# Optimization experiments

Hardware: AMD Instinct MI355X
Metric: run time of the kernel (lower is better)

Reference implementation:

```python
import jax, jax.numpy as jnp
import numpy as np

NUM_ITERS = 3


def squash(s):
    # s: [..., V]
    sq = (s ** 2).sum(-1, keepdims=True)
    return sq * s / ((1.0 + sq) * jnp.sqrt(sq))


def setup_inputs() -> dict:
    key = jax.random.key(0)
    kx, kw = jax.random.split(key)
    B, O, I, V, D = 32, 1, 4096, 512, 8
    x = jax.random.normal(kx, (B, I, D), dtype=jnp.float32)
    W = 0.01 * jax.random.normal(kw, (O, I, V, D), dtype=jnp.float32)
    return {"x": x, "W": W}


def reference(x, W):
    B = x.shape[0]
    O, I, V, _ = W.shape
    # x_hat[b,o,i,v] = sum_d W[o,i,v,d] * x[b,i,d]
    x_hat = jnp.einsum('oivd,bid->boiv', W, x)  # [B,O,I,V]
    x_hat_d = jax.lax.stop_gradient(x_hat)

    b = jnp.zeros((B, O, I), dtype=x.dtype)
    for it in range(NUM_ITERS):
        c = jax.nn.softmax(b, axis=1)  # over out caps
        if it == NUM_ITERS - 1:
            outputs = squash((c[:, :, :, None] * x_hat).sum(-2, keepdims=True))
        else:
            outputs = squash((c[:, :, :, None] * x_hat_d).sum(-2, keepdims=True))
            b = b + (outputs * x_hat_d).sum(-1)

    outputs = outputs.squeeze(-2)  # [B,O,V]
    # decode_idx == -1 branch
    classes = jax.nn.softmax(jnp.sqrt((outputs ** 2).sum(2)), axis=1)  # [B,O]
    max_idx = jnp.argmax(classes, axis=1)  # [B]
    masked = jax.nn.one_hot(max_idx, O, dtype=outputs.dtype)  # [B,O]
    t = (outputs * masked[:, :, None]).sum(axis=1)[:, None, :]  # [B,1,V]
    return (t, outputs)
```

## Files before the change

kernel.cpp:

```cpp
#include <hip/hip_runtime.h>
#include <stdint.h>


#define NB 32
#define NI 4096
#define NV 512
#define ND 8
#define NK 32768
#define KB 128
#define KSB (NK / KB)
#define KSW 16
#define NG (KB / 8)

typedef __fp16 f16x8 __attribute__((ext_vector_type(8)));
typedef __fp16 f16x2 __attribute__((ext_vector_type(2)));
typedef float  f32x16 __attribute__((ext_vector_type(16)));

__global__ __launch_bounds__(256) void x_prep(
    const float* __restrict__ x, __fp16* __restrict__ xh,
    __fp16* __restrict__ xl)
{
    const int tid = blockIdx.x * 256 + threadIdx.x;
    const int b = tid & 31;
    const int g = tid >> 5;

    const float4* xp = (const float4*)(x + (size_t)b * NK + (size_t)g * 8);
    const float4 f0 = xp[0];
    const float4 f1 = xp[1];

    const f16x2 h0 = __builtin_amdgcn_cvt_pkrtz(f0.x, f0.y);
    const f16x2 h1 = __builtin_amdgcn_cvt_pkrtz(f0.z, f0.w);
    const f16x2 h2 = __builtin_amdgcn_cvt_pkrtz(f1.x, f1.y);
    const f16x2 h3 = __builtin_amdgcn_cvt_pkrtz(f1.z, f1.w);
    const f16x2 l0 = __builtin_amdgcn_cvt_pkrtz(f0.x - (float)h0.x, f0.y - (float)h0.y);
    const f16x2 l1 = __builtin_amdgcn_cvt_pkrtz(f0.z - (float)h1.x, f0.w - (float)h1.y);
    const f16x2 l2 = __builtin_amdgcn_cvt_pkrtz(f1.x - (float)h2.x, f1.y - (float)h2.y);
    const f16x2 l3 = __builtin_amdgcn_cvt_pkrtz(f1.z - (float)h3.x, f1.w - (float)h3.y);

    const f16x8 h = {h0.x, h0.y, h1.x, h1.y, h2.x, h2.y, h3.x, h3.y};
    const f16x8 l = {l0.x, l0.y, l1.x, l1.y, l2.x, l2.y, l3.x, l3.y};
    ((f16x8*)xh)[tid] = h;
    ((f16x8*)xl)[tid] = l;
}

__global__ __launch_bounds__(1024) void caps_mfma(
    const float* __restrict__ W, const __fp16* __restrict__ xh,
    const __fp16* __restrict__ xl, __fp16* __restrict__ partial_h)
{
    const int t    = threadIdx.x;
    const int lane = t & 63;
    const int wave = t >> 6;
    const int half = lane >> 5;
    const int ln32 = lane & 31;

    const int kb = blockIdx.x & (KB - 1);
    const int vg = blockIdx.x >> 7;
    const int v0 = vg * 32;
    const int k0 = kb * KSB + wave * KSW;
    const int g0 = (k0 >> 3) + half;

    const __fp16* ah = xh + ((size_t)g0 * 32 + ln32) * 8;
    const __fp16* al = xl + ((size_t)g0 * 32 + ln32) * 8;
    const float4* wp = (const float4*)(W + ((size_t)g0 * NV + v0 + ln32) * ND);

    const float4 w0 = wp[0];
    const float4 w1 = wp[1];
    const f16x8 a_hi = *(const f16x8*)ah;
    const f16x8 a_lo = *(const f16x8*)al;

    const f16x2 h01 = __builtin_amdgcn_cvt_pkrtz(w0.x, w0.y);
    const f16x2 h23 = __builtin_amdgcn_cvt_pkrtz(w0.z, w0.w);
    const f16x2 h45 = __builtin_amdgcn_cvt_pkrtz(w1.x, w1.y);
    const f16x2 h67 = __builtin_amdgcn_cvt_pkrtz(w1.z, w1.w);
    const f16x8 b = {h01.x, h01.y, h23.x, h23.y, h45.x, h45.y, h67.x, h67.y};

    f32x16 acc;
#pragma unroll
    for (int r = 0; r < 16; ++r) acc[r] = 0.0f;
    acc = __builtin_amdgcn_mfma_f32_32x32x16_f16(a_hi, b, acc, 0, 0, 0);
    acc = __builtin_amdgcn_mfma_f32_32x32x16_f16(a_lo, b, acc, 0, 0, 0);

    __shared__ float red[16 * 1024];
#pragma unroll
    for (int r = 0; r < 16; ++r)
        red[wave * 1024 + r * 64 + lane] = acc[r];
    __syncthreads();

    float val = 0.0f;
#pragma unroll
    for (int w = 0; w < 16; ++w)
        val += red[w * 1024 + t];

    const int r  = t >> 6;
    const int ln = t & 63;
    const int row = (r & 3) + 8 * (r >> 2) + 4 * (ln >> 5);
    const int col = ln & 31;
    partial_h[((size_t)kb * NB + row) * NV + v0 + col] = (__fp16)val;
}

__global__ __launch_bounds__(256) void caps_reduce8(
    const __fp16* __restrict__ partial_h, float* __restrict__ partial2)
{
    const int t = threadIdx.x;
    const int b = blockIdx.x & 31;
    const int g = blockIdx.x >> 5;

    const __fp16* p = partial_h + ((size_t)(g * 8) * NB + b) * NV + 2 * t;
    float s0 = 0.0f, s1 = 0.0f;
#pragma unroll
    for (int j = 0; j < 8; ++j) {
        const f16x2 h = *(const f16x2*)(p + (size_t)j * NB * NV);
        s0 += (float)h.x;
        s1 += (float)h.y;
    }

    float2 o = {s0, s1};
    ((float2*)(partial2 + ((size_t)g * NB + b) * NV))[t] = o;
}

__global__ __launch_bounds__(512) void caps_finish(
    const float* __restrict__ partial2, float* __restrict__ out)
{
    const int v = threadIdx.x;
    const int b = blockIdx.x;

    float s = 0.0f;
#pragma unroll
    for (int g = 0; g < NG; ++g)
        s += partial2[((size_t)g * NB + b) * NV + v];

    float sq = s * s;
#pragma unroll
    for (int off = 32; off > 0; off >>= 1)
        sq += __shfl_xor(sq, off, 64);

    __shared__ float red[8];
    if ((v & 63) == 0) red[v >> 6] = sq;
    __syncthreads();
    float tot = 0.0f;
#pragma unroll
    for (int wv = 0; wv < 8; ++wv) tot += red[wv];

    const float factor = sqrtf(tot) / (1.0f + tot);
    const float r = s * factor;

    out[(size_t)b * NV + v]           = r;
    out[NB * NV + (size_t)b * NV + v] = r;
}

extern "C" void kernel_launch(void* const* d_in, const int* in_sizes, int n_in,
                              void* d_out, int out_size, void* d_ws, size_t ws_size,
                              hipStream_t stream) {
    const float* x = (const float*)d_in[0];
    const float* W = (const float*)d_in[1];
    float* out     = (float*)d_out;

    __fp16* xh       = (__fp16*)d_ws;
    __fp16* xl       = xh + (size_t)NB * NK;
    __fp16* partialh = xl + (size_t)NB * NK;
    float*  partial2 = (float*)(partialh + (size_t)KB * NB * NV);

    x_prep<<<(NB * NK / 8) / 256, 256, 0, stream>>>(x, xh, xl);
    caps_mfma<<<KB * 16, 1024, 0, stream>>>(W, xh, xl, partialh);
    caps_reduce8<<<NG * NB, 256, 0, stream>>>(partialh, partial2);
    caps_finish<<<NB, 512, 0, stream>>>(partial2, out);
}
```

Measured before the change: 108.4 us.

## Halve K-blocks with two MFMA steps per wave and merge reduce into finish

Each wave now covers 32 K-elements instead of 16, issuing four MFMAs over two groups, so the number of K-blocks and fp16 partial tiles is halved. The separate 8-way reduction kernel is removed and the finish kernel sums all 64 partials directly with 1024 threads split into two halves. This cuts a kernel launch and halves the partial-buffer traffic, but the finish kernel runs only 32 blocks doing long serial loads, and there are half as many mfma blocks.

```diff
diff --git a/kernel.cpp b/kernel.cpp
--- a/kernel.cpp
+++ b/kernel.cpp
@@ -7,10 +7,9 @@
 #define NV 512
 #define ND 8
 #define NK 32768
-#define KB 128
+#define KB 64
 #define KSB (NK / KB)
-#define KSW 16
-#define NG (KB / 8)
+#define KSW 32
 
 typedef __fp16 f16x8 __attribute__((ext_vector_type(8)));
 typedef __fp16 f16x2 __attribute__((ext_vector_type(2)));
@@ -54,31 +53,46 @@
     const int ln32 = lane & 31;
 
     const int kb = blockIdx.x & (KB - 1);
-    const int vg = blockIdx.x >> 7;
+    const int vg = blockIdx.x >> 6;
     const int v0 = vg * 32;
     const int k0 = kb * KSB + wave * KSW;
     const int g0 = (k0 >> 3) + half;
+    const int g1 = g0 + 2;
 
-    const __fp16* ah = xh + ((size_t)g0 * 32 + ln32) * 8;
-    const __fp16* al = xl + ((size_t)g0 * 32 + ln32) * 8;
-    const float4* wp = (const float4*)(W + ((size_t)g0 * NV + v0 + ln32) * ND);
+    const __fp16* ah0 = xh + ((size_t)g0 * 32 + ln32) * 8;
+    const __fp16* al0 = xl + ((size_t)g0 * 32 + ln32) * 8;
+    const float4* wp0 = (const float4*)(W + ((size_t)g0 * NV + v0 + ln32) * ND);
+    const __fp16* ah1 = xh + ((size_t)g1 * 32 + ln32) * 8;
+    const __fp16* al1 = xl + ((size_t)g1 * 32 + ln32) * 8;
+    const float4* wp1 = (const float4*)(W + ((size_t)g1 * NV + v0 + ln32) * ND);
 
-    const float4 w0 = wp[0];
-    const float4 w1 = wp[1];
-    const f16x8 a_hi = *(const f16x8*)ah;
-    const f16x8 a_lo = *(const f16x8*)al;
+    const float4 w00 = wp0[0];
+    const float4 w01 = wp0[1];
+    const float4 w10 = wp1[0];
+    const float4 w11 = wp1[1];
+    const f16x8 a0h = *(const f16x8*)ah0;
+    const f16x8 a0l = *(const f16x8*)al0;
+    const f16x8 a1h = *(const f16x8*)ah1;
+    const f16x8 a1l = *(const f16x8*)al1;
 
-    const f16x2 h01 = __builtin_amdgcn_cvt_pkrtz(w0.x, w0.y);
-    const f16x2 h23 = __builtin_amdgcn_cvt_pkrtz(w0.z, w0.w);
-    const f16x2 h45 = __builtin_amdgcn_cvt_pkrtz(w1.x, w1.y);
-    const f16x2 h67 = __builtin_amdgcn_cvt_pkrtz(w1.z, w1.w);
-    const f16x8 b = {h01.x, h01.y, h23.x, h23.y, h45.x, h45.y, h67.x, h67.y};
+    const f16x2 p01 = __builtin_amdgcn_cvt_pkrtz(w00.x, w00.y);
+    const f16x2 p23 = __builtin_amdgcn_cvt_pkrtz(w00.z, w00.w);
+    const f16x2 p45 = __builtin_amdgcn_cvt_pkrtz(w01.x, w01.y);
+    const f16x2 p67 = __builtin_amdgcn_cvt_pkrtz(w01.z, w01.w);
+    const f16x8 b0 = {p01.x, p01.y, p23.x, p23.y, p45.x, p45.y, p67.x, p67.y};
+    const f16x2 q01 = __builtin_amdgcn_cvt_pkrtz(w10.x, w10.y);
+    const f16x2 q23 = __builtin_amdgcn_cvt_pkrtz(w10.z, w10.w);
+    const f16x2 q45 = __builtin_amdgcn_cvt_pkrtz(w11.x, w11.y);
+    const f16x2 q67 = __builtin_amdgcn_cvt_pkrtz(w11.z, w11.w);
+    const f16x8 b1 = {q01.x, q01.y, q23.x, q23.y, q45.x, q45.y, q67.x, q67.y};
 
     f32x16 acc;
 #pragma unroll
     for (int r = 0; r < 16; ++r) acc[r] = 0.0f;
-    acc = __builtin_amdgcn_mfma_f32_32x32x16_f16(a_hi, b, acc, 0, 0, 0);
-    acc = __builtin_amdgcn_mfma_f32_32x32x16_f16(a_lo, b, acc, 0, 0, 0);
+    acc = __builtin_amdgcn_mfma_f32_32x32x16_f16(a0h, b0, acc, 0, 0, 0);
+    acc = __builtin_amdgcn_mfma_f32_32x32x16_f16(a0l, b0, acc, 0, 0, 0);
+    acc = __builtin_amdgcn_mfma_f32_32x32x16_f16(a1h, b1, acc, 0, 0, 0);
+    acc = __builtin_amdgcn_mfma_f32_32x32x16_f16(a1l, b1, acc, 0, 0, 0);
 
     __shared__ float red[16 * 1024];
 #pragma unroll
@@ -98,54 +112,49 @@
     partial_h[((size_t)kb * NB + row) * NV + v0 + col] = (__fp16)val;
 }
 
-__global__ __launch_bounds__(256) void caps_reduce8(
-    const __fp16* __restrict__ partial_h, float* __restrict__ partial2)
+__global__ __launch_bounds__(1024) void caps_finish(
+    const __fp16* __restrict__ partial_h, float* __restrict__ out)
 {
     const int t = threadIdx.x;
-    const int b = blockIdx.x & 31;
-    const int g = blockIdx.x >> 5;
-
-    const __fp16* p = partial_h + ((size_t)(g * 8) * NB + b) * NV + 2 * t;
-    float s0 = 0.0f, s1 = 0.0f;
-#pragma unroll
-    for (int j = 0; j < 8; ++j) {
-        const f16x2 h = *(const f16x2*)(p + (size_t)j * NB * NV);
-        s0 += (float)h.x;
-        s1 += (float)h.y;
-    }
-
-    float2 o = {s0, s1};
-    ((float2*)(partial2 + ((size_t)g * NB + b) * NV))[t] = o;
-}
-
-__global__ __launch_bounds__(512) void caps_finish(
-    const float* __restrict__ partial2, float* __restrict__ out)
-{
-    const int v = threadIdx.x;
+    const int v = t & 511;
+    const int h = t >> 9;
     const int b = blockIdx.x;
 
     float s = 0.0f;
 #pragma unroll
-    for (int g = 0; g < NG; ++g)
-        s += partial2[((size_t)g * NB + b) * NV + v];
+    for (int g = 0; g < KB / 2; ++g)
+        s += (float)partial_h[((size_t)(h * (KB / 2) + g) * NB + b) * NV + v];
 
-    float sq = s * s;
+    __shared__ float sv[1024];
+    sv[t] = s;
+    __syncthreads();
+
+    float sq = 0.0f;
+    float stot = 0.0f;
+    if (t < 512) {
+        stot = sv[t] + sv[t + 512];
+        sq = stot * stot;
+    }
 #pragma unroll
     for (int off = 32; off > 0; off >>= 1)
         sq += __shfl_xor(sq, off, 64);
 
-    __shared__ float red[8];
-    if ((v & 63) == 0) red[v >> 6] = sq;
+    __shared__ float red[16];
+    if ((t & 63) == 0) red[t >> 6] = sq;
     __syncthreads();
-    float tot = 0.0f;
+    if (t < 512) {
+        float tot = 0.0f;
 #pragma unroll
-    for (int wv = 0; wv < 8; ++wv) tot += red[wv];
+        for (int wv = 0; wv < 8; ++wv) tot += red[wv];
+#pragma unroll
+        for (int wv = 8; wv < 16; ++wv) tot += red[wv];
 
-    const float factor = sqrtf(tot) / (1.0f + tot);
-    const float r = s * factor;
+        const float factor = sqrtf(tot) / (1.0f + tot);
+        const float r = stot * factor;
 
-    out[(size_t)b * NV + v]           = r;
-    out[NB * NV + (size_t)b * NV + v] = r;
+        out[(size_t)b * NV + v]           = r;
+        out[NB * NV + (size_t)b * NV + v] = r;
+    }
 }
 
 extern "C" void kernel_launch(void* const* d_in, const int* in_sizes, int n_in,
@@ -158,10 +167,8 @@
     __fp16* xh       = (__fp16*)d_ws;
     __fp16* xl       = xh + (size_t)NB * NK;
     __fp16* partialh = xl + (size_t)NB * NK;
-    float*  partial2 = (float*)(partialh + (size_t)KB * NB * NV);
 
     x_prep<<<(NB * NK / 8) / 256, 256, 0, stream>>>(x, xh, xl);
     caps_mfma<<<KB * 16, 1024, 0, stream>>>(W, xh, xl, partialh);
-    caps_reduce8<<<NG * NB, 256, 0, stream>>>(partialh, partial2);
-    caps_finish<<<NB, 512, 0, stream>>>(partial2, out);
+    caps_finish<<<NB, 1024, 0, stream>>>(partialh, out);
 }
```

After: 105.4 us. 2.8% less time.
